# Optimization experiments

Measured on AMD Instinct MI355X. Metric: run time of the kernel, lower is better.

Reference implementation:

```python
import jax, jax.numpy as jnp
import numpy as np
from jax import lax

B, S, I, H, O, L = 64, 512, 512, 1024, 512, 2


def setup_inputs() -> dict:
    key = jax.random.key(0)
    ks = jax.random.split(key, 12)
    s_ih0 = 1.0 / np.sqrt(H)
    inp = {
        "x": jax.random.normal(ks[0], (B, S, I), dtype=jnp.float32),
        # PyTorch LSTM params: weight_ih_l{k} [4H, in], weight_hh_l{k} [4H, H], biases [4H]
        "W_ih0": jax.random.uniform(ks[1], (4 * H, I), minval=-s_ih0, maxval=s_ih0),
        "W_hh0": jax.random.uniform(ks[2], (4 * H, H), minval=-s_ih0, maxval=s_ih0),
        "b_ih0": jax.random.uniform(ks[3], (4 * H,), minval=-s_ih0, maxval=s_ih0),
        "b_hh0": jax.random.uniform(ks[4], (4 * H,), minval=-s_ih0, maxval=s_ih0),
        "W_ih1": jax.random.uniform(ks[5], (4 * H, H), minval=-s_ih0, maxval=s_ih0),
        "W_hh1": jax.random.uniform(ks[6], (4 * H, H), minval=-s_ih0, maxval=s_ih0),
        "b_ih1": jax.random.uniform(ks[7], (4 * H,), minval=-s_ih0, maxval=s_ih0),
        "b_hh1": jax.random.uniform(ks[8], (4 * H,), minval=-s_ih0, maxval=s_ih0),
        "W_fc": jax.random.uniform(ks[9], (O, H), minval=-s_ih0, maxval=s_ih0),
        "b_fc": jax.random.uniform(ks[10], (O,), minval=-s_ih0, maxval=s_ih0),
    }
    return inp


def lstm_layer(x, W_ih, W_hh, b_ih, b_hh):
    # x: [B, S, in]; zero initial h/c (module's init_hidden). Gate order i,f,g,o (PyTorch).
    b, s = x.shape[0], x.shape[1]
    h0 = jnp.zeros((b, H), dtype=x.dtype)
    c0 = jnp.zeros((b, H), dtype=x.dtype)
    # Precompute input contribution for all timesteps: [S, B, 4H]
    xg = jnp.einsum('bsi,gi->sbg', x, W_ih) + b_ih + b_hh

    def step(carry, xg_t):
        h, c = carry
        g = xg_t + h @ W_hh.T  # [B, 4H]
        i, f, gg, o = jnp.split(g, 4, axis=-1)
        i = jax.nn.sigmoid(i)
        f = jax.nn.sigmoid(f)
        gg = jnp.tanh(gg)
        o = jax.nn.sigmoid(o)
        c = f * c + i * gg
        h = o * jnp.tanh(c)
        return (h, c), h

    (h_n, c_n), ys = lax.scan(step, (h0, c0), xg)
    return jnp.swapaxes(ys, 0, 1), h_n, c_n  # [B, S, H]


def reference(x, W_ih0, W_hh0, b_ih0, b_hh0, W_ih1, W_hh1, b_ih1, b_hh1, W_fc, b_fc):
    y0, h0n, c0n = lstm_layer(x, W_ih0, W_hh0, b_ih0, b_hh0)
    y1, h1n, c1n = lstm_layer(y0, W_ih1, W_hh1, b_ih1, b_hh1)
    h_n = jnp.stack([h0n, h1n], axis=0)  # [L, B, H]
    c_n = jnp.stack([c0n, c1n], axis=0)
    out = y1.reshape(-1, H) @ W_fc.T + b_fc  # [B*S, O]
    return out, h_n, c_n
```

## Files before the change

kernel.cpp:

```cpp
#include <hip/hip_runtime.h>
#include <hip/hip_bf16.h>

#define B_   64
#define S_   512
#define I_   512
#define H_   1024
#define G4H  4096
#define O_   512
#define CH_  32
#define NCH  (S_ / CH_)

#define NBLK   256
#define THR_   512
#define LSTR   8
#define BARSTR 32

typedef short s16x8 __attribute__((ext_vector_type(8)));
typedef short s16x4 __attribute__((ext_vector_type(4)));
typedef float f32x4 __attribute__((ext_vector_type(4)));
typedef unsigned long long u64;
using bf16 = __hip_bfloat16;

__device__ __forceinline__ float bf2f(bf16 v) { return __bfloat162float(v); }
__device__ __forceinline__ bf16  f2bf(float f) { return __float2bfloat16(f); }
__device__ __forceinline__ short f2bfb(float f) { bf16 h = __float2bfloat16(f); return *(short*)&h; }

__device__ __forceinline__ void storeC(float* p, float v) { *p = v; }
__device__ __forceinline__ void storeC(bf16* p, float v)  { *p = f2bf(v); }

template <int AMAP, int CMAP, int ABF, typename CT>
__global__ __launch_bounds__(256) void gemm_bt(
    const void* __restrict__ Av, const float* __restrict__ Bw,
    CT* __restrict__ C,
    const float* __restrict__ bias1, const float* __restrict__ bias2,
    int M, int N, int K, int t0)
{
    __shared__ bf16 As[128 * 40];
    __shared__ bf16 Bs[128 * 40];

    const int tid  = threadIdx.x;
    const int wave = tid >> 6;
    const int lane = tid & 63;
    const int quad = lane >> 4;
    const int l16  = lane & 15;

    const int m_base = blockIdx.x * 128;
    const int n_base = blockIdx.y * 128;
    const int wm = (wave >> 1) * 64;
    const int wn = (wave & 1) * 64;

    f32x4 acc[4][4] = {};

    for (int k0 = 0; k0 < K; k0 += 32) {
        __syncthreads();
#pragma unroll
        for (int i = 0; i < 2; i++) {
            int l   = tid + i * 256;
            int row = l >> 2;
            int ko  = (l & 3) * 8;
            int m   = m_base + row;
            long ar = m;
            if (AMAP == 1) ar = (long)(m & 63) * S_ + t0 + (m >> 6);

            if (ABF) {
                const bf16* ap = (const bf16*)Av + ar * (long)K + k0 + ko;
                *(s16x8*)(&As[row * 40 + ko]) = *(const s16x8*)ap;
            } else {
                const float* ap = (const float*)Av + ar * (long)K + k0 + ko;
                f32x4 a0 = *(const f32x4*)ap;
                f32x4 a1 = *(const f32x4*)(ap + 4);
                s16x8 av;
#pragma unroll
                for (int j = 0; j < 4; j++) { av[j] = f2bfb(a0[j]); av[4 + j] = f2bfb(a1[j]); }
                *(s16x8*)(&As[row * 40 + ko]) = av;
            }

            const float* bp = &Bw[(long)(n_base + row) * K + k0 + ko];
            f32x4 b0 = *(const f32x4*)bp;
            f32x4 b1 = *(const f32x4*)(bp + 4);
            s16x8 bv;
#pragma unroll
            for (int j = 0; j < 4; j++) { bv[j] = f2bfb(b0[j]); bv[4 + j] = f2bfb(b1[j]); }
            *(s16x8*)(&Bs[row * 40 + ko]) = bv;
        }
        __syncthreads();

        s16x8 af[4], bfr[4];
#pragma unroll
        for (int i = 0; i < 4; i++)
            af[i] = *(const s16x8*)(&As[(wm + i * 16 + l16) * 40 + quad * 8]);
#pragma unroll
        for (int j = 0; j < 4; j++)
            bfr[j] = *(const s16x8*)(&Bs[(wn + j * 16 + l16) * 40 + quad * 8]);
#pragma unroll
        for (int i = 0; i < 4; i++)
#pragma unroll
            for (int j = 0; j < 4; j++)
                acc[i][j] = __builtin_amdgcn_mfma_f32_16x16x32_bf16(af[i], bfr[j], acc[i][j], 0, 0, 0);
    }

#pragma unroll
    for (int i = 0; i < 4; i++) {
#pragma unroll
        for (int j = 0; j < 4; j++) {
#pragma unroll
            for (int r = 0; r < 4; r++) {
                int m = m_base + wm + i * 16 + quad * 4 + r;
                int n = n_base + wn + j * 16 + l16;
                float v = acc[i][j][r];
                if (bias1) v += bias1[n];
                if (bias2) v += bias2[n];
                long cr = m;
                if (CMAP == 2) cr = (long)(m & 63) * S_ + t0 + (m >> 6);
                storeC(&C[cr * (long)N + n], v);
            }
        }
    }
}

__device__ __forceinline__ void grid_bar(unsigned* ctr, unsigned target)
{
    __syncthreads();
    const int t = threadIdx.x;
    if (t == 0)
        __hip_atomic_fetch_add(ctr + ((blockIdx.x & 127) & (LSTR - 1)) * BARSTR, 1u,
                               __ATOMIC_RELAXED, __HIP_MEMORY_SCOPE_AGENT);
    if (t < LSTR) {
        while (__hip_atomic_load(ctr + t * BARSTR, __ATOMIC_RELAXED,
                                 __HIP_MEMORY_SCOPE_AGENT) < target)
            __builtin_amdgcn_s_sleep(1);
    }
    __syncthreads();
}

__global__ __launch_bounds__(THR_, 1) void chunk_k(
    const bf16* __restrict__ xg0,
    const bf16* __restrict__ xg1,
    const float* __restrict__ Whh0,
    const float* __restrict__ Whh1,
    bf16* __restrict__ h0w,
    bf16* __restrict__ h1w,
    float* __restrict__ c0,
    float* __restrict__ c1,
    unsigned* __restrict__ bar,
    int cpar, int do0, int do1)
{
    const int layer  = blockIdx.x >> 7;
    const int nb     = blockIdx.x & 127;
    const int active = layer ? do1 : do0;
    if (!active) return;

    const bf16*  xg  = layer ? xg1  : xg0;
    const float* Whh = layer ? Whh1 : Whh0;
    float*       cst = layer ? c1   : c0;

    bf16 *rbuf, *cbuf;
    if (layer == 0) {
        rbuf = h0w + (size_t)(cpar & 1) * (CH_ + 1) * B_ * H_;
        cbuf = h0w + (size_t)((cpar + 1) & 1) * (CH_ + 1) * B_ * H_;
    } else {
        rbuf = h1w; cbuf = h1w;
    }

    const int tid  = threadIdx.x;
    const int lane = tid & 63;
    const int wave = tid >> 6;
    const int quad = lane >> 4;
    const int l16  = lane & 15;
    const int kw   = wave >> 2;
    const int mw   = wave & 3;

    unsigned* barL = bar + (size_t)layer * CH_ * LSTR * BARSTR;
    const unsigned bar_tgt =
        (layer ? (unsigned)cpar : (unsigned)(cpar + 1)) * (128 / LSTR);

    __shared__ bf16  wsh[32][1032];
    __shared__ float gs[2][64][36];

    {
        int r  = tid >> 4;
        int cc = (tid & 15) * 64;
        const float* src = Whh + ((long)(r >> 3) * H_ + nb * 8 + (r & 7)) * H_ + cc;
#pragma unroll
        for (int q = 0; q < 64; q += 4) {
            f32x4 v = *(const f32x4*)(src + q);
            s16x4 o;
#pragma unroll
            for (int w = 0; w < 4; w++) o[w] = f2bfb(v[w]);
            *(s16x4*)(&wsh[r][cc + q]) = o;
        }
    }
    __syncthreads();

    const int bb   = tid >> 3;
    const int uu   = tid & 7;
    const int unit = nb * 8 + uu;
    float creg = cst[(long)bb * H_ + unit];

    float xn[4];
#pragma unroll
    for (int g = 0; g < 4; g++)
        xn[g] = bf2f(xg[(long)bb * G4H + (long)g * H_ + unit]);

    for (int j = 0; j < CH_; j++) {
        const u64* ap = (const u64*)(rbuf + (long)j * (B_ * H_)
                       + (long)(mw * 16 + l16) * H_ + kw * 512) + quad * 2;
        u64 la[16], lb[16];
#pragma unroll
        for (int t = 0; t < 16; t++) {
            u64* p = (u64*)(ap + (size_t)t * 8);
            la[t] = __hip_atomic_load(p,     __ATOMIC_RELAXED, __HIP_MEMORY_SCOPE_AGENT);
            lb[t] = __hip_atomic_load(p + 1, __ATOMIC_RELAXED, __HIP_MEMORY_SCOPE_AGENT);
        }

        f32x4 acc0 = {}, acc1 = {};
#pragma unroll
        for (int t = 0; t < 16; t++) {
            union { u64 q[2]; s16x8 v; } ua;
            ua.q[0] = la[t]; ua.q[1] = lb[t];
            int k = kw * 512 + t * 32;
            s16x8 b0 = *(const s16x8*)(&wsh[l16][k + quad * 8]);
            s16x8 b1 = *(const s16x8*)(&wsh[16 + l16][k + quad * 8]);
            acc0 = __builtin_amdgcn_mfma_f32_16x16x32_bf16(ua.v, b0, acc0, 0, 0, 0);
            acc1 = __builtin_amdgcn_mfma_f32_16x16x32_bf16(ua.v, b1, acc1, 0, 0, 0);
        }

#pragma unroll
        for (int r = 0; r < 4; r++) {
            int m = mw * 16 + quad * 4 + r;
            gs[kw][m][l16]      = acc0[r];
            gs[kw][m][16 + l16] = acc1[r];
        }
        __syncthreads();

        {
            float gi = gs[0][bb][uu]      + gs[1][bb][uu]      + xn[0];
            float gf = gs[0][bb][8 + uu]  + gs[1][bb][8 + uu]  + xn[1];
            float gg = gs[0][bb][16 + uu] + gs[1][bb][16 + uu] + xn[2];
            float go = gs[0][bb][24 + uu] + gs[1][bb][24 + uu] + xn[3];

            float ig = 1.f / (1.f + __expf(-gi));
            float fg = 1.f / (1.f + __expf(-gf));
            float og = 1.f / (1.f + __expf(-go));
            float e2 = __expf(-2.f * fabsf(gg));
            float tg = (1.f - e2) / (1.f + e2);
            tg = (gg < 0.f) ? -tg : tg;

            creg = fg * creg + ig * tg;
            float e2c = __expf(-2.f * fabsf(creg));
            float tc = (1.f - e2c) / (1.f + e2c);
            tc = (creg < 0.f) ? -tc : tc;

            bf16 hv = f2bf(og * tc);
            unsigned my    = *(unsigned short*)&hv;
            unsigned other = (unsigned)__shfl((int)my, lane ^ 1, 64);
            if (!(uu & 1)) {
                unsigned v32 = my | (other << 16);
                unsigned* dst = (unsigned*)(rbuf + (long)(j + 1) * (B_ * H_)
                                + (long)bb * H_ + unit);
                __hip_atomic_store(dst, v32, __ATOMIC_RELAXED, __HIP_MEMORY_SCOPE_AGENT);
                if (j == CH_ - 1) {
                    unsigned* cd = (unsigned*)(cbuf + (long)bb * H_ + unit);
                    __hip_atomic_store(cd, v32, __ATOMIC_RELAXED, __HIP_MEMORY_SCOPE_AGENT);
                }
            }
        }

        if (j + 1 < CH_) {
            const bf16* xq = xg + (long)(j + 1) * (B_ * G4H);
#pragma unroll
            for (int g = 0; g < 4; g++)
                xn[g] = bf2f(xq[(long)bb * G4H + (long)g * H_ + unit]);
        }

        if (j < CH_ - 1)
            grid_bar(barL + (size_t)j * LSTR * BARSTR, bar_tgt);
    }

    cst[(long)bb * H_ + unit] = creg;
}

__global__ __launch_bounds__(256) void init_k(
    float* c0, float* c1, bf16* h0w, bf16* h1w, unsigned* bar, int nbar)
{
    int i = blockIdx.x * 256 + threadIdx.x;
    if (i < B_ * H_) {
        c0[i] = 0.f; c1[i] = 0.f;
        h0w[i] = f2bf(0.f);
        h1w[i] = f2bf(0.f);
    }
    if (i < nbar) bar[i] = 0u;
}

__global__ __launch_bounds__(256) void finalize_k(
    const bf16* __restrict__ h0w, const bf16* __restrict__ h1w,
    const float* __restrict__ c0, const float* __restrict__ c1,
    float* __restrict__ out_hn, float* __restrict__ out_cn)
{
    int i = blockIdx.x * 256 + threadIdx.x;
    if (i < B_ * H_) {
        out_hn[i]            = bf2f(h0w[i]);
        out_hn[B_ * H_ + i]  = bf2f(h1w[i]);
        out_cn[i]            = c0[i];
        out_cn[B_ * H_ + i]  = c1[i];
    }
}

extern "C" void kernel_launch(void* const* d_in, const int* in_sizes, int n_in,
                              void* d_out, int out_size, void* d_ws, size_t ws_size,
                              hipStream_t stream)
{
    const float* x    = (const float*)d_in[0];
    const float* Wih0 = (const float*)d_in[1];
    const float* Whh0 = (const float*)d_in[2];
    const float* bih0 = (const float*)d_in[3];
    const float* bhh0 = (const float*)d_in[4];
    const float* Wih1 = (const float*)d_in[5];
    const float* Whh1 = (const float*)d_in[6];
    const float* bih1 = (const float*)d_in[7];
    const float* bhh1 = (const float*)d_in[8];
    const float* Wfc  = (const float*)d_in[9];
    const float* bfc  = (const float*)d_in[10];
    float* out = (float*)d_out;

    char* p = (char*)d_ws;
    float* c0  = (float*)p; p += (size_t)B_ * H_ * 4;
    float* c1  = (float*)p; p += (size_t)B_ * H_ * 4;
    bf16* h0w  = (bf16*)p;  p += (size_t)2 * (CH_ + 1) * B_ * H_ * 2;
    bf16* h1w  = (bf16*)p;  p += (size_t)(CH_ + 1) * B_ * H_ * 2;
    bf16* xg0  = (bf16*)p;  p += (size_t)CH_ * B_ * G4H * 2;
    bf16* xg1  = (bf16*)p;  p += (size_t)CH_ * B_ * G4H * 2;
    unsigned* bar = (unsigned*)p;
    const int nbar = 2 * CH_ * LSTR * BARSTR;
    p += (size_t)nbar * 4;

    init_k<<<(B_ * H_ + 255) / 256, 256, 0, stream>>>(c0, c1, h0w, h1w, bar, nbar);

    const dim3 gxg0((B_ * CH_) / 128, G4H / 128);
    const dim3 gfc((B_ * CH_) / 128, O_ / 128);

    for (int c = 0; c <= NCH; c++) {
        const int do0 = (c < NCH);
        const int do1 = (c >= 1);

        if (do0) {
            gemm_bt<1, 0, 0, bf16><<<gxg0, 256, 0, stream>>>(
                x, Wih0, xg0, bih0, bhh0, B_ * CH_, G4H, I_, c * CH_);
        }
        if (do1) {
            const bf16* h0chunk = h0w + (size_t)((c - 1) & 1) * (CH_ + 1) * B_ * H_ + B_ * H_;
            gemm_bt<0, 0, 1, bf16><<<gxg0, 256, 0, stream>>>(
                h0chunk, Wih1, xg1, bih1, bhh1, B_ * CH_, G4H, H_, 0);
        }

        {
            const bf16*  a0  = xg0;  const bf16*  a1  = xg1;
            const float* w0  = Whh0; const float* w1  = Whh1;
            bf16* hp0 = h0w; bf16* hp1 = h1w;
            float* cp0 = c0; float* cp1 = c1;
            unsigned* bp = bar;
            int cv = c, d0 = do0, d1 = do1;
            void* args[] = { &a0, &a1, &w0, &w1, &hp0, &hp1,
                             &cp0, &cp1, &bp, &cv, &d0, &d1 };
            hipLaunchCooperativeKernel((const void*)chunk_k,
                                       dim3(NBLK), dim3(THR_), args, 0, stream);
        }

        if (do1) {
            gemm_bt<0, 2, 1, float><<<gfc, 256, 0, stream>>>(
                h1w + B_ * H_, Wfc, out, bfc, (const float*)nullptr,
                B_ * CH_, O_, H_, (c - 1) * CH_);
        }
    }

    finalize_k<<<(B_ * H_ + 255) / 256, 256, 0, stream>>>(
        h0w, h1w, c0, c1,
        out + (size_t)B_ * S_ * O_,
        out + (size_t)B_ * S_ * O_ + 2 * (size_t)B_ * H_);
}
```

Before: 8.141 ms.

## Halve recurrent grid to 128 blocks with 16 hidden units per block

Each persistent LSTM recurrence block now owns 16 hidden units (64 gate columns) instead of 8, so the grid drops from 256 to 128 blocks, 64 per layer. Weights in LDS double to 64 rows, each wave runs four MFMA column tiles, and the K-split partial sums are combined in shared memory in two phases. Each thread handles two batch rows of the gate math. The aim is to halve the participants in every per-timestep grid barrier and the redundant loads of h per step. The cost is more serial work per block and larger LDS use, about 132KB for the weight tile.

```diff
diff --git a/kernel.cpp b/kernel.cpp
--- a/kernel.cpp
+++ b/kernel.cpp
@@ -10,7 +10,7 @@
 #define CH_  32
 #define NCH  (S_ / CH_)
 
-#define NBLK   256
+#define NBLK   128
 #define THR_   512
 #define LSTR   8
 #define BARSTR 32
@@ -123,7 +123,7 @@
     __syncthreads();
     const int t = threadIdx.x;
     if (t == 0)
-        __hip_atomic_fetch_add(ctr + ((blockIdx.x & 127) & (LSTR - 1)) * BARSTR, 1u,
+        __hip_atomic_fetch_add(ctr + ((blockIdx.x & 63) & (LSTR - 1)) * BARSTR, 1u,
                                __ATOMIC_RELAXED, __HIP_MEMORY_SCOPE_AGENT);
     if (t < LSTR) {
         while (__hip_atomic_load(ctr + t * BARSTR, __ATOMIC_RELAXED,
@@ -145,8 +145,8 @@
     unsigned* __restrict__ bar,
     int cpar, int do0, int do1)
 {
-    const int layer  = blockIdx.x >> 7;
-    const int nb     = blockIdx.x & 127;
+    const int layer  = blockIdx.x >> 6;
+    const int nb     = blockIdx.x & 63;
     const int active = layer ? do1 : do0;
     if (!active) return;
 
@@ -172,17 +172,17 @@
 
     unsigned* barL = bar + (size_t)layer * CH_ * LSTR * BARSTR;
     const unsigned bar_tgt =
-        (layer ? (unsigned)cpar : (unsigned)(cpar + 1)) * (128 / LSTR);
-
-    __shared__ bf16  wsh[32][1032];
-    __shared__ float gs[2][64][36];
+        (layer ? (unsigned)cpar : (unsigned)(cpar + 1)) * (64 / LSTR);
+
+    __shared__ bf16  wsh[64][1032];
+    __shared__ float gs[64][68];
 
     {
-        int r  = tid >> 4;
-        int cc = (tid & 15) * 64;
-        const float* src = Whh + ((long)(r >> 3) * H_ + nb * 8 + (r & 7)) * H_ + cc;
-#pragma unroll
-        for (int q = 0; q < 64; q += 4) {
+        int r  = tid >> 3;
+        int cc = (tid & 7) * 128;
+        const float* src = Whh + ((long)(r >> 4) * H_ + nb * 16 + (r & 15)) * H_ + cc;
+#pragma unroll
+        for (int q = 0; q < 128; q += 4) {
             f32x4 v = *(const f32x4*)(src + q);
             s16x4 o;
 #pragma unroll
@@ -192,15 +192,23 @@
     }
     __syncthreads();
 
-    const int bb   = tid >> 3;
-    const int uu   = tid & 7;
-    const int unit = nb * 8 + uu;
-    float creg = cst[(long)bb * H_ + unit];
-
-    float xn[4];
-#pragma unroll
-    for (int g = 0; g < 4; g++)
-        xn[g] = bf2f(xg[(long)bb * G4H + (long)g * H_ + unit]);
+    const int uu   = tid & 15;
+    const int unit = nb * 16 + uu;
+    float creg[2];
+#pragma unroll
+    for (int rep = 0; rep < 2; rep++) {
+        int bb = (tid + rep * 512) >> 4;
+        creg[rep] = cst[(long)bb * H_ + unit];
+    }
+
+    float xn[2][4];
+#pragma unroll
+    for (int rep = 0; rep < 2; rep++) {
+        int bb = (tid + rep * 512) >> 4;
+#pragma unroll
+        for (int g = 0; g < 4; g++)
+            xn[rep][g] = bf2f(xg[(long)bb * G4H + (long)g * H_ + unit]);
+    }
 
     for (int j = 0; j < CH_; j++) {
         const u64* ap = (const u64*)(rbuf + (long)j * (B_ * H_)
@@ -213,31 +221,44 @@
             lb[t] = __hip_atomic_load(p + 1, __ATOMIC_RELAXED, __HIP_MEMORY_SCOPE_AGENT);
         }
 
-        f32x4 acc0 = {}, acc1 = {};
+        f32x4 acc[4] = {};
 #pragma unroll
         for (int t = 0; t < 16; t++) {
             union { u64 q[2]; s16x8 v; } ua;
             ua.q[0] = la[t]; ua.q[1] = lb[t];
             int k = kw * 512 + t * 32;
-            s16x8 b0 = *(const s16x8*)(&wsh[l16][k + quad * 8]);
-            s16x8 b1 = *(const s16x8*)(&wsh[16 + l16][k + quad * 8]);
-            acc0 = __builtin_amdgcn_mfma_f32_16x16x32_bf16(ua.v, b0, acc0, 0, 0, 0);
-            acc1 = __builtin_amdgcn_mfma_f32_16x16x32_bf16(ua.v, b1, acc1, 0, 0, 0);
-        }
-
-#pragma unroll
-        for (int r = 0; r < 4; r++) {
-            int m = mw * 16 + quad * 4 + r;
-            gs[kw][m][l16]      = acc0[r];
-            gs[kw][m][16 + l16] = acc1[r];
+#pragma unroll
+            for (int cf = 0; cf < 4; cf++) {
+                s16x8 b = *(const s16x8*)(&wsh[cf * 16 + l16][k + quad * 8]);
+                acc[cf] = __builtin_amdgcn_mfma_f32_16x16x32_bf16(ua.v, b, acc[cf], 0, 0, 0);
+            }
+        }
+
+        if (kw == 0) {
+#pragma unroll
+            for (int cf = 0; cf < 4; cf++)
+#pragma unroll
+                for (int r = 0; r < 4; r++)
+                    gs[mw * 16 + quad * 4 + r][cf * 16 + l16] = acc[cf][r];
         }
         __syncthreads();
-
-        {
-            float gi = gs[0][bb][uu]      + gs[1][bb][uu]      + xn[0];
-            float gf = gs[0][bb][8 + uu]  + gs[1][bb][8 + uu]  + xn[1];
-            float gg = gs[0][bb][16 + uu] + gs[1][bb][16 + uu] + xn[2];
-            float go = gs[0][bb][24 + uu] + gs[1][bb][24 + uu] + xn[3];
+        if (kw == 1) {
+#pragma unroll
+            for (int cf = 0; cf < 4; cf++)
+#pragma unroll
+                for (int r = 0; r < 4; r++)
+                    gs[mw * 16 + quad * 4 + r][cf * 16 + l16] += acc[cf][r];
+        }
+        __syncthreads();
+
+        unsigned short hb[2];
+#pragma unroll
+        for (int rep = 0; rep < 2; rep++) {
+            int bb = (tid + rep * 512) >> 4;
+            float gi = gs[bb][uu]      + xn[rep][0];
+            float gf = gs[bb][16 + uu] + xn[rep][1];
+            float gg = gs[bb][32 + uu] + xn[rep][2];
+            float go = gs[bb][48 + uu] + xn[rep][3];
 
             float ig = 1.f / (1.f + __expf(-gi));
             float fg = 1.f / (1.f + __expf(-gf));
@@ -246,13 +267,18 @@
             float tg = (1.f - e2) / (1.f + e2);
             tg = (gg < 0.f) ? -tg : tg;
 
-            creg = fg * creg + ig * tg;
-            float e2c = __expf(-2.f * fabsf(creg));
+            creg[rep] = fg * creg[rep] + ig * tg;
+            float e2c = __expf(-2.f * fabsf(creg[rep]));
             float tc = (1.f - e2c) / (1.f + e2c);
-            tc = (creg < 0.f) ? -tc : tc;
+            tc = (creg[rep] < 0.f) ? -tc : tc;
 
             bf16 hv = f2bf(og * tc);
-            unsigned my    = *(unsigned short*)&hv;
+            hb[rep] = *(unsigned short*)&hv;
+        }
+#pragma unroll
+        for (int rep = 0; rep < 2; rep++) {
+            int bb = (tid + rep * 512) >> 4;
+            unsigned my    = hb[rep];
             unsigned other = (unsigned)__shfl((int)my, lane ^ 1, 64);
             if (!(uu & 1)) {
                 unsigned v32 = my | (other << 16);
@@ -269,15 +295,23 @@
         if (j + 1 < CH_) {
             const bf16* xq = xg + (long)(j + 1) * (B_ * G4H);
 #pragma unroll
-            for (int g = 0; g < 4; g++)
-                xn[g] = bf2f(xq[(long)bb * G4H + (long)g * H_ + unit]);
+            for (int rep = 0; rep < 2; rep++) {
+                int bb = (tid + rep * 512) >> 4;
+#pragma unroll
+                for (int g = 0; g < 4; g++)
+                    xn[rep][g] = bf2f(xq[(long)bb * G4H + (long)g * H_ + unit]);
+            }
         }
 
         if (j < CH_ - 1)
             grid_bar(barL + (size_t)j * LSTR * BARSTR, bar_tgt);
     }
 
-    cst[(long)bb * H_ + unit] = creg;
+#pragma unroll
+    for (int rep = 0; rep < 2; rep++) {
+        int bb = (tid + rep * 512) >> 4;
+        cst[(long)bb * H_ + unit] = creg[rep];
+    }
 }
 
 __global__ __launch_bounds__(256) void init_k(
```

Result: no change. 8.125 ms (-0.2%).
